# Kernel optimization log

Measured on AMD Instinct MI355X. Metric: run time of the kernel, lower is better.

Reference implementation:

```python
import jax, jax.numpy as jnp
import numpy as np

SIGMA = 1.0
DELTA = 1.0
TOPK = 10
TOPK_HALF = int(np.around(TOPK / 2))  # 5
EPS = 1e-12


def _cdist(a, b):
    # Euclidean distance matrix, grad-safe sqrt at zero (matches torch.cdist values).
    d2 = (jnp.sum(a * a, axis=1)[:, None]
          + jnp.sum(b * b, axis=1)[None, :]
          - 2.0 * (a @ b.T))
    d2 = jnp.maximum(d2, 0.0)
    pos = d2 > 0.0
    return jnp.where(pos, jnp.sqrt(jnp.where(pos, d2, 1.0)), 0.0)


def _consistency_weights(t_emb):
    # Everything here is under torch.no_grad() in the original.
    N = t_emb.shape[0]
    T_dist = _cdist(t_emb, t_emb)
    W_P = jnp.exp(-(T_dist ** 2) / SIGMA)
    _, idx = jax.lax.top_k(W_P, TOPK)                      # [N, TOPK]
    rows = jnp.arange(N)[:, None]
    W_NN = jnp.zeros_like(W_P).at[rows, idx].set(1.0)      # scatter_ ones
    V = (((W_NN + W_NN.T) / 2) == 1.0).astype(W_P.dtype)   # mutual kNN (symmetric)
    # Vectorized form of the per-row python loop:
    #   W_C_tilda[i, j] = V[i, j] * (sum_k V[i, k] * V[j, k]) / sum_k V[i, k]
    deg = jnp.sum(V, axis=1)                               # >= 1 (self is always a NN)
    overlap = V @ V.T                                      # [N, N] neighbor overlap
    W_C_tilda = V * overlap / deg[:, None]
    topk_half_index = idx[:, :TOPK_HALF]                   # [N, TOPK_HALF]
    W_C_hat = jnp.mean(W_C_tilda[topk_half_index], axis=1) # gather rows, mean -> [N, N]
    W_C = (W_C_hat + W_C_hat.T) / 2
    return (W_P + W_C) / 2


def reference(s_emb, t_emb):
    # disable_mu = 0 -> s_emb NOT normalized; t_emb always normalized.
    t_norm = t_emb / jnp.maximum(
        jnp.linalg.norm(t_emb, axis=1, keepdims=True), EPS)
    N = s_emb.shape[0]
    S_dist = _cdist(s_emb, s_emb)
    S_dist = S_dist / jnp.mean(S_dist, axis=1, keepdims=True)
    W = jax.lax.stop_gradient(_consistency_weights(t_norm))
    off_diag = 1.0 - jnp.eye(N, dtype=W.dtype)
    pos_weight = W * off_diag
    neg_weight = (1.0 - W) * off_diag
    pull = jnp.maximum(S_dist, 0.0) ** 2 * pos_weight
    push = jnp.maximum(DELTA - S_dist, 0.0) ** 2 * neg_weight
    return (jnp.sum(pull) + jnp.sum(push)) / (N * (N - 1))


def setup_inputs() -> dict:
    key = jax.random.key(0)
    k1, k2 = jax.random.split(key)
    N, D = 2048, 1024
    return {
        "s_emb": jax.random.normal(k1, (N, D), dtype=jnp.float32),
        "t_emb": jax.random.normal(k2, (N, D), dtype=jnp.float32),
    }
```

## Files before the change

### kernel.cpp

```cpp
#include <hip/hip_runtime.h>
#include <math.h>

#define N_ 2048
#define D_ 1024
#define TOPK 10
#define TOPK_HALF 5
#define INV_NORM (1.0f / ((float)N_ * (float)(N_ - 1)))

typedef __attribute__((ext_vector_type(8))) short short8;
typedef __attribute__((ext_vector_type(4))) float floatx4;

__device__ __forceinline__ short f2bf(float f) {
  unsigned u = __float_as_uint(f);
  unsigned r = (u + 0x7fffu + ((u >> 16) & 1u)) >> 16;
  return (short)r;
}
__device__ __forceinline__ float bf2f(short b) {
  return __uint_as_float(((unsigned)(unsigned short)b) << 16);
}

__device__ __forceinline__ void gld_lds16(const short* g, short* l) {
  __builtin_amdgcn_global_load_lds(
      (const __attribute__((address_space(1))) unsigned int*)(g),
      (__attribute__((address_space(3))) unsigned int*)(l), 16, 0, 0);
}

#define BAR() asm volatile("s_barrier" ::: "memory")
#define WAIT4_BAR() asm volatile("s_waitcnt vmcnt(4)\ns_barrier" ::: "memory")
#define WAIT0_BAR() asm volatile("s_waitcnt vmcnt(0)\ns_barrier" ::: "memory")

__global__ __launch_bounds__(256) void prep_kernel(const float* __restrict__ t,
                                                   const float* __restrict__ s,
                                                   short* __restrict__ tb,
                                                   short* __restrict__ sb,
                                                   float* __restrict__ tt,
                                                   float* __restrict__ ss,
                                                   float* __restrict__ rowsum,
                                                   float* __restrict__ out) {
  int b = blockIdx.x, tid = threadIdx.x;
  __shared__ float red[256];
  if (b == 0) {
    for (int j = tid; j < N_; j += 256) rowsum[j] = 0.f;
    if (tid == 0) out[0] = 0.f;
  }
  if (b < N_) {
    const float4* rp = (const float4*)(t + (size_t)b * D_);
    float4 v = rp[tid];
    red[tid] = v.x * v.x + v.y * v.y + v.z * v.z + v.w * v.w;
    __syncthreads();
    for (int st = 128; st > 0; st >>= 1) { if (tid < st) red[tid] += red[tid + st]; __syncthreads(); }
    float inv = 1.f / fmaxf(sqrtf(red[0]), 1e-12f);
    __syncthreads();
    float a = v.x * inv, bb = v.y * inv, c = v.z * inv, d = v.w * inv;
    uint2 pk;
    pk.x = (unsigned)(unsigned short)f2bf(a) | ((unsigned)(unsigned short)f2bf(bb) << 16);
    pk.y = (unsigned)(unsigned short)f2bf(c) | ((unsigned)(unsigned short)f2bf(d) << 16);
    ((uint2*)(tb + (size_t)b * D_))[tid] = pk;
    red[tid] = a * a + bb * bb + c * c + d * d;
    __syncthreads();
    for (int st = 128; st > 0; st >>= 1) { if (tid < st) red[tid] += red[tid + st]; __syncthreads(); }
    if (tid == 0) tt[b] = red[0];
  } else {
    int row = b - N_;
    const float4* rp = (const float4*)(s + (size_t)row * D_);
    float4 v = rp[tid];
    uint2 pk;
    pk.x = (unsigned)(unsigned short)f2bf(v.x) | ((unsigned)(unsigned short)f2bf(v.y) << 16);
    pk.y = (unsigned)(unsigned short)f2bf(v.z) | ((unsigned)(unsigned short)f2bf(v.w) << 16);
    ((uint2*)(sb + (size_t)row * D_))[tid] = pk;
    red[tid] = v.x * v.x + v.y * v.y + v.z * v.z + v.w * v.w;
    __syncthreads();
    for (int st = 128; st > 0; st >>= 1) { if (tid < st) red[tid] += red[tid + st]; __syncthreads(); }
    if (tid == 0) ss[row] = red[0];
  }
}

#define NTRI 528
__global__ __launch_bounds__(256) void gram_sym_kernel(
    const short* __restrict__ Tb, const short* __restrict__ Sb,
    const float* __restrict__ tt, const float* __restrict__ ss,
    short* __restrict__ WPb, short* __restrict__ Sob,
    float* __restrict__ rowsum) {
  int p = blockIdx.x;
  const int mode = (p >= NTRI);
  int q = p - mode * NTRI;
  int bi = (int)((sqrtf(8.f * (float)q + 1.f) - 1.f) * 0.5f);
  if (bi > 31) bi = 31;
  while ((bi + 1) * (bi + 2) / 2 <= q) bi++;
  while (bi * (bi + 1) / 2 > q) bi--;
  int bj = q - bi * (bi + 1) / 2;

  const short* A = mode ? Sb : Tb;
  const float* rn = mode ? ss : tt;
  short* outb = mode ? Sob : WPb;

  __shared__ __align__(16) short smem[4 * 4096];

  int tid = threadIdx.x;
  int w = tid >> 6, lane = tid & 63;
  int i0 = bi * 64, j0 = bj * 64;
  int wr = w >> 1, wc = w & 1;
  int quad = lane >> 4, l16 = lane & 15;

  floatx4 acc[2][2] = {};

  int sr8 = lane >> 3;
  int gch = ((lane & 7) ^ sr8) * 8;
  const short* Ag = A + (size_t)(i0 + w * 16 + sr8) * D_ + gch;
  const short* Bg = A + (size_t)(j0 + w * 16 + sr8) * D_ + gch;
  int lloc = (w * 16 + sr8) * 64 + (lane & 7) * 8;

#define STAGE(buf, k0)                                                   \
  do {                                                                   \
    short* Al = smem + (buf)*8192 + lloc;                                \
    short* Bl = smem + (buf)*8192 + 4096 + lloc;                         \
    gld_lds16(Ag + (k0), Al);                                            \
    gld_lds16(Ag + (k0) + (size_t)8 * D_, Al + 512);                     \
    gld_lds16(Bg + (k0), Bl);                                            \
    gld_lds16(Bg + (k0) + (size_t)8 * D_, Bl + 512);                     \
  } while (0)

  STAGE(0, 0);
#pragma unroll 2
  for (int it = 0; it < 16; it++) {
    int cur = it & 1;
    if (it) BAR();
    if (it < 15) {
      STAGE(!cur, (it + 1) * 64);
      WAIT4_BAR();
    } else {
      WAIT0_BAR();
    }
    const short* Ab = smem + cur * 8192;
    const short* Bb = smem + cur * 8192 + 4096;
#pragma unroll
    for (int ks = 0; ks < 64; ks += 32) {
      int cb = ks >> 3;
      short8 af[2], bfr[2];
#pragma unroll
      for (int mt = 0; mt < 2; mt++) {
        int rr = wr * 32 + mt * 16 + l16;
        af[mt] = *(const short8*)&Ab[rr * 64 + (((cb + quad) ^ (l16 & 7)) << 3)];
      }
#pragma unroll
      for (int nt = 0; nt < 2; nt++) {
        int rr = wc * 32 + nt * 16 + l16;
        bfr[nt] = *(const short8*)&Bb[rr * 64 + (((cb + quad) ^ (l16 & 7)) << 3)];
      }
#pragma unroll
      for (int mt = 0; mt < 2; mt++)
#pragma unroll
        for (int nt = 0; nt < 2; nt++)
          acc[mt][nt] = __builtin_amdgcn_mfma_f32_16x16x32_bf16(af[mt], bfr[nt], acc[mt][nt], 0, 0, 0);
    }
  }

  float ov[2][2][4];
#pragma unroll
  for (int mt = 0; mt < 2; mt++) {
#pragma unroll
    for (int r = 0; r < 4; r++) {
      int i = i0 + wr * 32 + mt * 16 + quad * 4 + r;
      float ri = rn[i];
      float rs = 0.f;
#pragma unroll
      for (int nt = 0; nt < 2; nt++) {
        int j = j0 + wc * 32 + nt * 16 + l16;
        float d2 = fmaxf(ri + rn[j] - 2.f * acc[mt][nt][r], 0.f);
        float o = mode ? sqrtf(d2) : expf(-d2);
        if (i == j) o = mode ? 0.f : 1.f;
        ov[mt][nt][r] = o;
        outb[(size_t)i * N_ + j] = f2bf(o);
        rs += o;
      }
      if (mode) {
        rs += __shfl_xor(rs, 1); rs += __shfl_xor(rs, 2);
        rs += __shfl_xor(rs, 4); rs += __shfl_xor(rs, 8);
        if (l16 == 0) atomicAdd(&rowsum[i], rs);
      }
    }
  }

  if (bi != bj) {
    if (mode) {
#pragma unroll
      for (int nt = 0; nt < 2; nt++) {
        float cs = 0.f;
#pragma unroll
        for (int mt = 0; mt < 2; mt++)
#pragma unroll
          for (int r = 0; r < 4; r++) cs += ov[mt][nt][r];
        cs += __shfl_xor(cs, 16);
        cs += __shfl_xor(cs, 32);
        if (quad == 0) atomicAdd(&rowsum[j0 + wc * 32 + nt * 16 + l16], cs);
      }
    }
    BAR();
    float* fs = (float*)smem + w * 1088;
#pragma unroll
    for (int mt = 0; mt < 2; mt++)
#pragma unroll
      for (int nt = 0; nt < 2; nt++)
#pragma unroll
        for (int r = 0; r < 4; r++) {
          int lr = mt * 16 + quad * 4 + r;
          int lc = nt * 16 + l16;
          fs[lc * 34 + lr] = ov[mt][nt][r];
        }
#pragma unroll
    for (int itx = 0; itx < 8; itx++) {
      int sidx = itx * 64 + lane;
      int lc = sidx >> 4;
      int k2 = (sidx & 15) * 2;
      float lo = fs[lc * 34 + k2];
      float hi = fs[lc * 34 + k2 + 1];
      unsigned pk = (unsigned)(unsigned short)f2bf(lo) |
                    ((unsigned)(unsigned short)f2bf(hi) << 16);
      size_t jg = (size_t)(j0 + wc * 32 + lc);
      *(unsigned*)(outb + jg * N_ + i0 + wr * 32 + k2) = pk;
    }
  }
}

__global__ __launch_bounds__(64) void topk_loss_kernel(const short* __restrict__ WPb,
                                                       const short* __restrict__ Sb,
                                                       const float* __restrict__ rowsum,
                                                       int* __restrict__ idx,
                                                       unsigned* __restrict__ mask,
                                                       float* __restrict__ out) {
  int row = blockIdx.x, lane = threadIdx.x;
  const short8* wpr = (const short8*)(WPb + (size_t)row * N_);
  const short8* sr = (const short8*)(Sb + (size_t)row * N_);
  float rminv = (float)N_ / rowsum[row];
  float w[32];
  float local = 0.f;
#pragma unroll
  for (int c4 = 0; c4 < 4; c4++) {
    short8 wp8 = wpr[lane * 4 + c4];
    short8 s8 = sr[lane * 4 + c4];
#pragma unroll
    for (int e = 0; e < 8; e++) {
      float wv = bf2f(wp8[e]);
      w[c4 * 8 + e] = wv;
      float sv = bf2f(s8[e]) * rminv;
      float d = fmaxf(1.f - sv, 0.f);
      local += d * d + 0.5f * wv * (sv * sv - d * d);
    }
  }
#pragma unroll
  for (int off = 32; off > 0; off >>= 1) local += __shfl_down(local, off);
  if (lane == 0) {
    atomicAdd(out, (local - 0.5f) * INV_NORM);
    mask[row] = 0u;
  }
  int base = lane * 32;
  int sel[TOPK];
  for (int t = 0; t < TOPK; t++) {
    float bv = -2.f; int bi = 0;
#pragma unroll
    for (int c = 0; c < 32; c++)
      if (w[c] > bv) { bv = w[c]; bi = base + c; }
#pragma unroll
    for (int off = 32; off > 0; off >>= 1) {
      float ovv = __shfl_down(bv, off);
      int oi = __shfl_down(bi, off);
      if (ovv > bv || (ovv == bv && oi < bi)) { bv = ovv; bi = oi; }
    }
    bi = __shfl(bi, 0);
    sel[t] = bi;
    bool mine = (bi >> 5) == lane;
    int cc = bi & 31;
#pragma unroll
    for (int c = 0; c < 32; c++)
      if (mine && cc == c) w[c] = -1.f;
  }
  if (lane == 0) {
#pragma unroll
    for (int t = 0; t < TOPK; t++) idx[row * TOPK + t] = sel[t];
  }
}

__global__ __launch_bounds__(256) void mutual_kernel(const int* __restrict__ idx,
                                                     unsigned* __restrict__ mask) {
  int t = blockIdx.x * 256 + threadIdx.x;
  int i = t >> 4, k = t & 15;
  if (i >= N_ || k >= TOPK) return;
  int j = idx[i * TOPK + k];
  bool mut = false;
#pragma unroll
  for (int l = 0; l < TOPK; l++) mut |= (idx[j * TOPK + l] == i);
  if (mut) atomicOr(&mask[i], 1u << k);
}

__global__ __launch_bounds__(256) void sparse_wc_kernel(
    const int* __restrict__ idx, const unsigned* __restrict__ mask,
    const short* __restrict__ Sb, const float* __restrict__ rowsum,
    float* __restrict__ out) {
  int t = blockIdx.x * 256 + threadIdx.x;
  int i = t >> 6, r = t & 63;
  float contrib = 0.f;
  if (i < N_ && r < TOPK_HALF * TOPK) {
    int mi = r / TOPK, k = r - mi * TOPK;
    int m = idx[i * TOPK + mi];
    unsigned mm = mask[m];
    if ((mm >> k) & 1u) {
      int col = idx[m * TOPK + k];
      if (col != i) {
        int dm = __popc(mm);
        unsigned mc = mask[col];
        int jm[TOPK], jc[TOPK];
#pragma unroll
        for (int l = 0; l < TOPK; l++) jm[l] = idx[m * TOPK + l];
#pragma unroll
        for (int l = 0; l < TOPK; l++) jc[l] = idx[col * TOPK + l];
        int c = 0;
#pragma unroll
        for (int a = 0; a < TOPK; a++) {
          if ((mm >> a) & 1u) {
            int na = jm[a];
#pragma unroll
            for (int b = 0; b < TOPK; b++) c += (((mc >> b) & 1u) && (jc[b] == na));
          }
        }
        float v = (float)c / (float)dm * 0.1f;
        float s1 = bf2f(Sb[(size_t)i * N_ + col]) * ((float)N_ / rowsum[i]);
        float d1 = fmaxf(1.f - s1, 0.f);
        float s2 = bf2f(Sb[(size_t)col * N_ + i]) * ((float)N_ / rowsum[col]);
        float d2 = fmaxf(1.f - s2, 0.f);
        contrib = 0.5f * v * ((s1 * s1 - d1 * d1) + (s2 * s2 - d2 * d2));
      }
    }
  }
  __shared__ float red[256];
  red[threadIdx.x] = contrib; __syncthreads();
  for (int st = 128; st > 0; st >>= 1) {
    if (threadIdx.x < st) red[threadIdx.x] += red[threadIdx.x + st];
    __syncthreads();
  }
  if (threadIdx.x == 0) atomicAdd(out, red[0] * INV_NORM);
}

extern "C" void kernel_launch(void* const* d_in, const int* in_sizes, int n_in,
                              void* d_out, int out_size, void* d_ws, size_t ws_size,
                              hipStream_t stream) {
  const float* s_emb = (const float*)d_in[0];
  const float* t_emb = (const float*)d_in[1];
  float* out = (float*)d_out;

  const size_t NN = (size_t)N_ * N_;
  const size_t ND = (size_t)N_ * D_;
  short* t_bf = (short*)d_ws;
  short* s_bf = t_bf + ND;
  short* WPb = s_bf + ND;
  short* Sb = WPb + NN;
  float* tt = (float*)(Sb + NN);
  float* ss = tt + N_;
  float* rowsum = ss + N_;
  int* idx = (int*)(rowsum + N_);
  unsigned* mask = (unsigned*)(idx + (size_t)N_ * TOPK);

  prep_kernel<<<2 * N_, 256, 0, stream>>>(t_emb, s_emb, t_bf, s_bf, tt, ss, rowsum, out);

  gram_sym_kernel<<<2 * NTRI, 256, 0, stream>>>(t_bf, s_bf, tt, ss, WPb, Sb, rowsum);

  topk_loss_kernel<<<N_, 64, 0, stream>>>(WPb, Sb, rowsum, idx, mask, out);
  mutual_kernel<<<N_ * 16 / 256, 256, 0, stream>>>(idx, mask);
  sparse_wc_kernel<<<N_ * 64 / 256, 256, 0, stream>>>(idx, mask, Sb, rowsum, out);
}
```

Baseline: 141.3 us.

## Fuse all stages into one cooperative persistent kernel with grid syncs

Replaces the five separate launches (prep, symmetric gram, topk/loss, mutual, sparse WC) with a single cooperative kernel that loops over the work of each phase and separates phases with grid.sync. The prep phase now uses one wave per row with shuffle reductions instead of shared-memory tree reductions. The aim is to remove per-launch overhead and the tail gaps between kernels. In exchange it caps the grid at up to 1024 blocks, adds the cost of the grid barriers, and leaves the topk phase using only 2 of 4 waves per block.

```diff
diff --git a/kernel.cpp b/kernel.cpp
--- a/kernel.cpp
+++ b/kernel.cpp
@@ -1,10 +1,14 @@
 #include <hip/hip_runtime.h>
+#include <hip/hip_cooperative_groups.h>
 #include <math.h>
+
+namespace cg = cooperative_groups;
 
 #define N_ 2048
 #define D_ 1024
 #define TOPK 10
 #define TOPK_HALF 5
+#define NTRI 528
 #define INV_NORM (1.0f / ((float)N_ * (float)(N_ - 1)))
 
 typedef __attribute__((ext_vector_type(8))) short short8;
@@ -29,315 +33,315 @@
 #define WAIT4_BAR() asm volatile("s_waitcnt vmcnt(4)\ns_barrier" ::: "memory")
 #define WAIT0_BAR() asm volatile("s_waitcnt vmcnt(0)\ns_barrier" ::: "memory")
 
-__global__ __launch_bounds__(256) void prep_kernel(const float* __restrict__ t,
-                                                   const float* __restrict__ s,
-                                                   short* __restrict__ tb,
-                                                   short* __restrict__ sb,
-                                                   float* __restrict__ tt,
-                                                   float* __restrict__ ss,
-                                                   float* __restrict__ rowsum,
-                                                   float* __restrict__ out) {
-  int b = blockIdx.x, tid = threadIdx.x;
-  __shared__ float red[256];
-  if (b == 0) {
+__global__ __launch_bounds__(256, 4) void mega_kernel(
+    const float* __restrict__ t, const float* __restrict__ s,
+    short* __restrict__ tb, short* __restrict__ sb,
+    float* __restrict__ tt, float* __restrict__ ss,
+    float* __restrict__ rowsum, int* __restrict__ idx,
+    unsigned* __restrict__ mask,
+    short* __restrict__ WPb, short* __restrict__ Sob,
+    float* __restrict__ out) {
+  cg::grid_group grid = cg::this_grid();
+  __shared__ __align__(16) short smem[4 * 4096];
+  int tid = threadIdx.x, w = tid >> 6, lane = tid & 63;
+
+  if (blockIdx.x == 0) {
     for (int j = tid; j < N_; j += 256) rowsum[j] = 0.f;
     if (tid == 0) out[0] = 0.f;
   }
-  if (b < N_) {
-    const float4* rp = (const float4*)(t + (size_t)b * D_);
-    float4 v = rp[tid];
-    red[tid] = v.x * v.x + v.y * v.y + v.z * v.z + v.w * v.w;
+  if (blockIdx.x == 1 % gridDim.x) {
+    for (int j = tid; j < N_; j += 256) mask[j] = 0u;
+  }
+  for (int row = blockIdx.x * 4 + w; row < 2 * N_; row += gridDim.x * 4) {
+    if (row < N_) {
+      const float4* rp = (const float4*)(t + (size_t)row * D_);
+      float4 v[4];
+      float acc = 0.f;
+#pragma unroll
+      for (int c4 = 0; c4 < 4; c4++) {
+        v[c4] = rp[lane + 64 * c4];
+        acc += v[c4].x * v[c4].x + v[c4].y * v[c4].y + v[c4].z * v[c4].z + v[c4].w * v[c4].w;
+      }
+#pragma unroll
+      for (int off = 1; off < 64; off <<= 1) acc += __shfl_xor(acc, off);
+      float inv = 1.f / fmaxf(sqrtf(acc), 1e-12f);
+      float s2 = 0.f;
+#pragma unroll
+      for (int c4 = 0; c4 < 4; c4++) {
+        float a = v[c4].x * inv, b = v[c4].y * inv, c = v[c4].z * inv, d = v[c4].w * inv;
+        uint2 pk;
+        pk.x = (unsigned)(unsigned short)f2bf(a) | ((unsigned)(unsigned short)f2bf(b) << 16);
+        pk.y = (unsigned)(unsigned short)f2bf(c) | ((unsigned)(unsigned short)f2bf(d) << 16);
+        ((uint2*)(tb + (size_t)row * D_))[lane + 64 * c4] = pk;
+        s2 += a * a + b * b + c * c + d * d;
+      }
+#pragma unroll
+      for (int off = 1; off < 64; off <<= 1) s2 += __shfl_xor(s2, off);
+      if (lane == 0) tt[row] = s2;
+    } else {
+      int r2 = row - N_;
+      const float4* rp = (const float4*)(s + (size_t)r2 * D_);
+      float acc = 0.f;
+#pragma unroll
+      for (int c4 = 0; c4 < 4; c4++) {
+        float4 v = rp[lane + 64 * c4];
+        uint2 pk;
+        pk.x = (unsigned)(unsigned short)f2bf(v.x) | ((unsigned)(unsigned short)f2bf(v.y) << 16);
+        pk.y = (unsigned)(unsigned short)f2bf(v.z) | ((unsigned)(unsigned short)f2bf(v.w) << 16);
+        ((uint2*)(sb + (size_t)r2 * D_))[lane + 64 * c4] = pk;
+        acc += v.x * v.x + v.y * v.y + v.z * v.z + v.w * v.w;
+      }
+#pragma unroll
+      for (int off = 1; off < 64; off <<= 1) acc += __shfl_xor(acc, off);
+      if (lane == 0) ss[r2] = acc;
+    }
+  }
+  grid.sync();
+
+  for (int p = blockIdx.x; p < 2 * NTRI; p += gridDim.x) {
     __syncthreads();
-    for (int st = 128; st > 0; st >>= 1) { if (tid < st) red[tid] += red[tid + st]; __syncthreads(); }
-    float inv = 1.f / fmaxf(sqrtf(red[0]), 1e-12f);
+    const int mode = (p >= NTRI);
+    int q = p - mode * NTRI;
+    int bi = (int)((sqrtf(8.f * (float)q + 1.f) - 1.f) * 0.5f);
+    if (bi > 31) bi = 31;
+    while ((bi + 1) * (bi + 2) / 2 <= q) bi++;
+    while (bi * (bi + 1) / 2 > q) bi--;
+    int bj = q - bi * (bi + 1) / 2;
+
+    const short* A = mode ? sb : tb;
+    const float* rn = mode ? ss : tt;
+    short* outb = mode ? Sob : WPb;
+
+    int i0 = bi * 64, j0 = bj * 64;
+    int wr = w >> 1, wc = w & 1;
+    int quad = lane >> 4, l16 = lane & 15;
+    floatx4 acc[2][2] = {};
+
+    int sr8 = lane >> 3;
+    int gch = ((lane & 7) ^ sr8) * 8;
+    const short* Ag = A + (size_t)(i0 + w * 16 + sr8) * D_ + gch;
+    const short* Bg = A + (size_t)(j0 + w * 16 + sr8) * D_ + gch;
+    int lloc = (w * 16 + sr8) * 64 + (lane & 7) * 8;
+
+#define STAGE(buf, k0)                                       \
+  do {                                                       \
+    short* Al = smem + (buf)*8192 + lloc;                    \
+    short* Bl = smem + (buf)*8192 + 4096 + lloc;             \
+    gld_lds16(Ag + (k0), Al);                                \
+    gld_lds16(Ag + (k0) + (size_t)8 * D_, Al + 512);         \
+    gld_lds16(Bg + (k0), Bl);                                \
+    gld_lds16(Bg + (k0) + (size_t)8 * D_, Bl + 512);         \
+  } while (0)
+
+    STAGE(0, 0);
+#pragma unroll 2
+    for (int it = 0; it < 16; it++) {
+      int cur = it & 1;
+      if (it) BAR();
+      if (it < 15) {
+        STAGE(!cur, (it + 1) * 64);
+        WAIT4_BAR();
+      } else {
+        WAIT0_BAR();
+      }
+      const short* Ab = smem + cur * 8192;
+      const short* Bb = smem + cur * 8192 + 4096;
+#pragma unroll
+      for (int ks = 0; ks < 64; ks += 32) {
+        int cb = ks >> 3;
+        short8 af[2], bfr[2];
+#pragma unroll
+        for (int mt = 0; mt < 2; mt++) {
+          int rr = wr * 32 + mt * 16 + l16;
+          af[mt] = *(const short8*)&Ab[rr * 64 + (((cb + quad) ^ (l16 & 7)) << 3)];
+        }
+#pragma unroll
+        for (int nt = 0; nt < 2; nt++) {
+          int rr = wc * 32 + nt * 16 + l16;
+          bfr[nt] = *(const short8*)&Bb[rr * 64 + (((cb + quad) ^ (l16 & 7)) << 3)];
+        }
+#pragma unroll
+        for (int mt = 0; mt < 2; mt++)
+#pragma unroll
+          for (int nt = 0; nt < 2; nt++)
+            acc[mt][nt] = __builtin_amdgcn_mfma_f32_16x16x32_bf16(af[mt], bfr[nt], acc[mt][nt], 0, 0, 0);
+      }
+    }
+
+    float ov[2][2][4];
+#pragma unroll
+    for (int mt = 0; mt < 2; mt++) {
+#pragma unroll
+      for (int r = 0; r < 4; r++) {
+        int i = i0 + wr * 32 + mt * 16 + quad * 4 + r;
+        float ri = rn[i];
+        float rs = 0.f;
+#pragma unroll
+        for (int nt = 0; nt < 2; nt++) {
+          int j = j0 + wc * 32 + nt * 16 + l16;
+          float d2 = fmaxf(ri + rn[j] - 2.f * acc[mt][nt][r], 0.f);
+          float o = mode ? sqrtf(d2) : expf(-d2);
+          if (i == j) o = mode ? 0.f : 1.f;
+          ov[mt][nt][r] = o;
+          outb[(size_t)i * N_ + j] = f2bf(o);
+          rs += o;
+        }
+        if (mode) {
+          rs += __shfl_xor(rs, 1); rs += __shfl_xor(rs, 2);
+          rs += __shfl_xor(rs, 4); rs += __shfl_xor(rs, 8);
+          if (l16 == 0) atomicAdd(&rowsum[i], rs);
+        }
+      }
+    }
+
+    if (bi != bj) {
+      if (mode) {
+#pragma unroll
+        for (int nt = 0; nt < 2; nt++) {
+          float cs = 0.f;
+#pragma unroll
+          for (int mt = 0; mt < 2; mt++)
+#pragma unroll
+            for (int r = 0; r < 4; r++) cs += ov[mt][nt][r];
+          cs += __shfl_xor(cs, 16);
+          cs += __shfl_xor(cs, 32);
+          if (quad == 0) atomicAdd(&rowsum[j0 + wc * 32 + nt * 16 + l16], cs);
+        }
+      }
+      BAR();
+      float* fs = (float*)smem + w * 1088;
+#pragma unroll
+      for (int mt = 0; mt < 2; mt++)
+#pragma unroll
+        for (int nt = 0; nt < 2; nt++)
+#pragma unroll
+          for (int r = 0; r < 4; r++)
+            fs[(nt * 16 + l16) * 34 + mt * 16 + quad * 4 + r] = ov[mt][nt][r];
+#pragma unroll
+      for (int itx = 0; itx < 8; itx++) {
+        int sidx = itx * 64 + lane;
+        int lc = sidx >> 4;
+        int k2 = (sidx & 15) * 2;
+        float lo = fs[lc * 34 + k2];
+        float hi = fs[lc * 34 + k2 + 1];
+        unsigned pk = (unsigned)(unsigned short)f2bf(lo) |
+                      ((unsigned)(unsigned short)f2bf(hi) << 16);
+        size_t jg = (size_t)(j0 + wc * 32 + lc);
+        *(unsigned*)(outb + jg * N_ + i0 + wr * 32 + k2) = pk;
+      }
+    }
+  }
+  grid.sync();
+
+  if (w < 2) {
+    for (int row = blockIdx.x * 2 + w; row < N_; row += gridDim.x * 2) {
+      const short8* wpr = (const short8*)(WPb + (size_t)row * N_);
+      const short8* sr = (const short8*)(Sob + (size_t)row * N_);
+      float rminv = (float)N_ / rowsum[row];
+      float wreg[32];
+      float local = 0.f;
+#pragma unroll
+      for (int c4 = 0; c4 < 4; c4++) {
+        short8 wp8 = wpr[lane * 4 + c4];
+        short8 s8 = sr[lane * 4 + c4];
+#pragma unroll
+        for (int e = 0; e < 8; e++) {
+          float wv = bf2f(wp8[e]);
+          wreg[c4 * 8 + e] = wv;
+          float sv = bf2f(s8[e]) * rminv;
+          float d = fmaxf(1.f - sv, 0.f);
+          local += d * d + 0.5f * wv * (sv * sv - d * d);
+        }
+      }
+#pragma unroll
+      for (int off = 32; off > 0; off >>= 1) local += __shfl_down(local, off);
+      if (lane == 0) atomicAdd(out, (local - 0.5f) * INV_NORM);
+      int base = lane * 32;
+      int sel[TOPK];
+      for (int tq = 0; tq < TOPK; tq++) {
+        float bv = -2.f; int bi = 0;
+#pragma unroll
+        for (int c = 0; c < 32; c++)
+          if (wreg[c] > bv) { bv = wreg[c]; bi = base + c; }
+#pragma unroll
+        for (int off = 32; off > 0; off >>= 1) {
+          float ovv = __shfl_down(bv, off);
+          int oi = __shfl_down(bi, off);
+          if (ovv > bv || (ovv == bv && oi < bi)) { bv = ovv; bi = oi; }
+        }
+        bi = __shfl(bi, 0);
+        sel[tq] = bi;
+        bool mine = (bi >> 5) == lane;
+        int cc = bi & 31;
+#pragma unroll
+        for (int c = 0; c < 32; c++)
+          if (mine && cc == c) wreg[c] = -1.f;
+      }
+      if (lane == 0) {
+#pragma unroll
+        for (int tq = 0; tq < TOPK; tq++) idx[row * TOPK + tq] = sel[tq];
+      }
+    }
+  }
+  grid.sync();
+
+  for (int tk = blockIdx.x * 256 + tid; tk < N_ * 16; tk += gridDim.x * 256) {
+    int i = tk >> 4, k = tk & 15;
+    if (k < TOPK) {
+      int j = idx[i * TOPK + k];
+      bool mut = false;
+#pragma unroll
+      for (int l = 0; l < TOPK; l++) mut |= (idx[j * TOPK + l] == i);
+      if (mut) atomicOr(&mask[i], 1u << k);
+    }
+  }
+  grid.sync();
+
+  float contrib = 0.f;
+  for (int tk = blockIdx.x * 256 + tid; tk < N_ * 64; tk += gridDim.x * 256) {
+    int i = tk >> 6, r = tk & 63;
+    if (r < TOPK_HALF * TOPK) {
+      int mi = r / TOPK, k = r - mi * TOPK;
+      int m = idx[i * TOPK + mi];
+      unsigned mm = mask[m];
+      if ((mm >> k) & 1u) {
+        int col = idx[m * TOPK + k];
+        if (col != i) {
+          int dm = __popc(mm);
+          unsigned mc = mask[col];
+          int jm[TOPK], jc[TOPK];
+#pragma unroll
+          for (int l = 0; l < TOPK; l++) jm[l] = idx[m * TOPK + l];
+#pragma unroll
+          for (int l = 0; l < TOPK; l++) jc[l] = idx[col * TOPK + l];
+          int c = 0;
+#pragma unroll
+          for (int a = 0; a < TOPK; a++) {
+            if ((mm >> a) & 1u) {
+              int na = jm[a];
+#pragma unroll
+              for (int b = 0; b < TOPK; b++) c += (((mc >> b) & 1u) && (jc[b] == na));
+            }
+          }
+          float v = (float)c / (float)dm * 0.1f;
+          float s1 = bf2f(Sob[(size_t)i * N_ + col]) * ((float)N_ / rowsum[i]);
+          float d1 = fmaxf(1.f - s1, 0.f);
+          float s2 = bf2f(Sob[(size_t)col * N_ + i]) * ((float)N_ / rowsum[col]);
+          float d2 = fmaxf(1.f - s2, 0.f);
+          contrib += 0.5f * v * ((s1 * s1 - d1 * d1) + (s2 * s2 - d2 * d2));
+        }
+      }
+    }
+  }
+  __syncthreads();
+  float* red = (float*)smem;
+  red[tid] = contrib;
+  __syncthreads();
+  for (int st = 128; st > 0; st >>= 1) {
+    if (tid < st) red[tid] += red[tid + st];
     __syncthreads();
-    float a = v.x * inv, bb = v.y * inv, c = v.z * inv, d = v.w * inv;
-    uint2 pk;
-    pk.x = (unsigned)(unsigned short)f2bf(a) | ((unsigned)(unsigned short)f2bf(bb) << 16);
-    pk.y = (unsigned)(unsigned short)f2bf(c) | ((unsigned)(unsigned short)f2bf(d) << 16);
-    ((uint2*)(tb + (size_t)b * D_))[tid] = pk;
-    red[tid] = a * a + bb * bb + c * c + d * d;
-    __syncthreads();
-    for (int st = 128; st > 0; st >>= 1) { if (tid < st) red[tid] += red[tid + st]; __syncthreads(); }
-    if (tid == 0) tt[b] = red[0];
-  } else {
-    int row = b - N_;
-    const float4* rp = (const float4*)(s + (size_t)row * D_);
-    float4 v = rp[tid];
-    uint2 pk;
-    pk.x = (unsigned)(unsigned short)f2bf(v.x) | ((unsigned)(unsigned short)f2bf(v.y) << 16);
-    pk.y = (unsigned)(unsigned short)f2bf(v.z) | ((unsigned)(unsigned short)f2bf(v.w) << 16);
-    ((uint2*)(sb + (size_t)row * D_))[tid] = pk;
-    red[tid] = v.x * v.x + v.y * v.y + v.z * v.z + v.w * v.w;
-    __syncthreads();
-    for (int st = 128; st > 0; st >>= 1) { if (tid < st) red[tid] += red[tid + st]; __syncthreads(); }
-    if (tid == 0) ss[row] = red[0];
-  }
-}
-
-#define NTRI 528
-__global__ __launch_bounds__(256) void gram_sym_kernel(
-    const short* __restrict__ Tb, const short* __restrict__ Sb,
-    const float* __restrict__ tt, const float* __restrict__ ss,
-    short* __restrict__ WPb, short* __restrict__ Sob,
-    float* __restrict__ rowsum) {
-  int p = blockIdx.x;
-  const int mode = (p >= NTRI);
-  int q = p - mode * NTRI;
-  int bi = (int)((sqrtf(8.f * (float)q + 1.f) - 1.f) * 0.5f);
-  if (bi > 31) bi = 31;
-  while ((bi + 1) * (bi + 2) / 2 <= q) bi++;
-  while (bi * (bi + 1) / 2 > q) bi--;
-  int bj = q - bi * (bi + 1) / 2;
-
-  const short* A = mode ? Sb : Tb;
-  const float* rn = mode ? ss : tt;
-  short* outb = mode ? Sob : WPb;
-
-  __shared__ __align__(16) short smem[4 * 4096];
-
-  int tid = threadIdx.x;
-  int w = tid >> 6, lane = tid & 63;
-  int i0 = bi * 64, j0 = bj * 64;
-  int wr = w >> 1, wc = w & 1;
-  int quad = lane >> 4, l16 = lane & 15;
-
-  floatx4 acc[2][2] = {};
-
-  int sr8 = lane >> 3;
-  int gch = ((lane & 7) ^ sr8) * 8;
-  const short* Ag = A + (size_t)(i0 + w * 16 + sr8) * D_ + gch;
-  const short* Bg = A + (size_t)(j0 + w * 16 + sr8) * D_ + gch;
-  int lloc = (w * 16 + sr8) * 64 + (lane & 7) * 8;
-
-#define STAGE(buf, k0)                                                   \
-  do {                                                                   \
-    short* Al = smem + (buf)*8192 + lloc;                                \
-    short* Bl = smem + (buf)*8192 + 4096 + lloc;                         \
-    gld_lds16(Ag + (k0), Al);                                            \
-    gld_lds16(Ag + (k0) + (size_t)8 * D_, Al + 512);                     \
-    gld_lds16(Bg + (k0), Bl);                                            \
-    gld_lds16(Bg + (k0) + (size_t)8 * D_, Bl + 512);                     \
-  } while (0)
-
-  STAGE(0, 0);
-#pragma unroll 2
-  for (int it = 0; it < 16; it++) {
-    int cur = it & 1;
-    if (it) BAR();
-    if (it < 15) {
-      STAGE(!cur, (it + 1) * 64);
-      WAIT4_BAR();
-    } else {
-      WAIT0_BAR();
-    }
-    const short* Ab = smem + cur * 8192;
-    const short* Bb = smem + cur * 8192 + 4096;
-#pragma unroll
-    for (int ks = 0; ks < 64; ks += 32) {
-      int cb = ks >> 3;
-      short8 af[2], bfr[2];
-#pragma unroll
-      for (int mt = 0; mt < 2; mt++) {
-        int rr = wr * 32 + mt * 16 + l16;
-        af[mt] = *(const short8*)&Ab[rr * 64 + (((cb + quad) ^ (l16 & 7)) << 3)];
-      }
-#pragma unroll
-      for (int nt = 0; nt < 2; nt++) {
-        int rr = wc * 32 + nt * 16 + l16;
-        bfr[nt] = *(const short8*)&Bb[rr * 64 + (((cb + quad) ^ (l16 & 7)) << 3)];
-      }
-#pragma unroll
-      for (int mt = 0; mt < 2; mt++)
-#pragma unroll
-        for (int nt = 0; nt < 2; nt++)
-          acc[mt][nt] = __builtin_amdgcn_mfma_f32_16x16x32_bf16(af[mt], bfr[nt], acc[mt][nt], 0, 0, 0);
-    }
-  }
-
-  float ov[2][2][4];
-#pragma unroll
-  for (int mt = 0; mt < 2; mt++) {
-#pragma unroll
-    for (int r = 0; r < 4; r++) {
-      int i = i0 + wr * 32 + mt * 16 + quad * 4 + r;
-      float ri = rn[i];
-      float rs = 0.f;
-#pragma unroll
-      for (int nt = 0; nt < 2; nt++) {
-        int j = j0 + wc * 32 + nt * 16 + l16;
-        float d2 = fmaxf(ri + rn[j] - 2.f * acc[mt][nt][r], 0.f);
-        float o = mode ? sqrtf(d2) : expf(-d2);
-        if (i == j) o = mode ? 0.f : 1.f;
-        ov[mt][nt][r] = o;
-        outb[(size_t)i * N_ + j] = f2bf(o);
-        rs += o;
-      }
-      if (mode) {
-        rs += __shfl_xor(rs, 1); rs += __shfl_xor(rs, 2);
-        rs += __shfl_xor(rs, 4); rs += __shfl_xor(rs, 8);
-        if (l16 == 0) atomicAdd(&rowsum[i], rs);
-      }
-    }
-  }
-
-  if (bi != bj) {
-    if (mode) {
-#pragma unroll
-      for (int nt = 0; nt < 2; nt++) {
-        float cs = 0.f;
-#pragma unroll
-        for (int mt = 0; mt < 2; mt++)
-#pragma unroll
-          for (int r = 0; r < 4; r++) cs += ov[mt][nt][r];
-        cs += __shfl_xor(cs, 16);
-        cs += __shfl_xor(cs, 32);
-        if (quad == 0) atomicAdd(&rowsum[j0 + wc * 32 + nt * 16 + l16], cs);
-      }
-    }
-    BAR();
-    float* fs = (float*)smem + w * 1088;
-#pragma unroll
-    for (int mt = 0; mt < 2; mt++)
-#pragma unroll
-      for (int nt = 0; nt < 2; nt++)
-#pragma unroll
-        for (int r = 0; r < 4; r++) {
-          int lr = mt * 16 + quad * 4 + r;
-          int lc = nt * 16 + l16;
-          fs[lc * 34 + lr] = ov[mt][nt][r];
-        }
-#pragma unroll
-    for (int itx = 0; itx < 8; itx++) {
-      int sidx = itx * 64 + lane;
-      int lc = sidx >> 4;
-      int k2 = (sidx & 15) * 2;
-      float lo = fs[lc * 34 + k2];
-      float hi = fs[lc * 34 + k2 + 1];
-      unsigned pk = (unsigned)(unsigned short)f2bf(lo) |
-                    ((unsigned)(unsigned short)f2bf(hi) << 16);
-      size_t jg = (size_t)(j0 + wc * 32 + lc);
-      *(unsigned*)(outb + jg * N_ + i0 + wr * 32 + k2) = pk;
-    }
-  }
-}
-
-__global__ __launch_bounds__(64) void topk_loss_kernel(const short* __restrict__ WPb,
-                                                       const short* __restrict__ Sb,
-                                                       const float* __restrict__ rowsum,
-                                                       int* __restrict__ idx,
-                                                       unsigned* __restrict__ mask,
-                                                       float* __restrict__ out) {
-  int row = blockIdx.x, lane = threadIdx.x;
-  const short8* wpr = (const short8*)(WPb + (size_t)row * N_);
-  const short8* sr = (const short8*)(Sb + (size_t)row * N_);
-  float rminv = (float)N_ / rowsum[row];
-  float w[32];
-  float local = 0.f;
-#pragma unroll
-  for (int c4 = 0; c4 < 4; c4++) {
-    short8 wp8 = wpr[lane * 4 + c4];
-    short8 s8 = sr[lane * 4 + c4];
-#pragma unroll
-    for (int e = 0; e < 8; e++) {
-      float wv = bf2f(wp8[e]);
-      w[c4 * 8 + e] = wv;
-      float sv = bf2f(s8[e]) * rminv;
-      float d = fmaxf(1.f - sv, 0.f);
-      local += d * d + 0.5f * wv * (sv * sv - d * d);
-    }
-  }
-#pragma unroll
-  for (int off = 32; off > 0; off >>= 1) local += __shfl_down(local, off);
-  if (lane == 0) {
-    atomicAdd(out, (local - 0.5f) * INV_NORM);
-    mask[row] = 0u;
-  }
-  int base = lane * 32;
-  int sel[TOPK];
-  for (int t = 0; t < TOPK; t++) {
-    float bv = -2.f; int bi = 0;
-#pragma unroll
-    for (int c = 0; c < 32; c++)
-      if (w[c] > bv) { bv = w[c]; bi = base + c; }
-#pragma unroll
-    for (int off = 32; off > 0; off >>= 1) {
-      float ovv = __shfl_down(bv, off);
-      int oi = __shfl_down(bi, off);
-      if (ovv > bv || (ovv == bv && oi < bi)) { bv = ovv; bi = oi; }
-    }
-    bi = __shfl(bi, 0);
-    sel[t] = bi;
-    bool mine = (bi >> 5) == lane;
-    int cc = bi & 31;
-#pragma unroll
-    for (int c = 0; c < 32; c++)
-      if (mine && cc == c) w[c] = -1.f;
-  }
-  if (lane == 0) {
-#pragma unroll
-    for (int t = 0; t < TOPK; t++) idx[row * TOPK + t] = sel[t];
-  }
-}
-
-__global__ __launch_bounds__(256) void mutual_kernel(const int* __restrict__ idx,
-                                                     unsigned* __restrict__ mask) {
-  int t = blockIdx.x * 256 + threadIdx.x;
-  int i = t >> 4, k = t & 15;
-  if (i >= N_ || k >= TOPK) return;
-  int j = idx[i * TOPK + k];
-  bool mut = false;
-#pragma unroll
-  for (int l = 0; l < TOPK; l++) mut |= (idx[j * TOPK + l] == i);
-  if (mut) atomicOr(&mask[i], 1u << k);
-}
-
-__global__ __launch_bounds__(256) void sparse_wc_kernel(
-    const int* __restrict__ idx, const unsigned* __restrict__ mask,
-    const short* __restrict__ Sb, const float* __restrict__ rowsum,
-    float* __restrict__ out) {
-  int t = blockIdx.x * 256 + threadIdx.x;
-  int i = t >> 6, r = t & 63;
-  float contrib = 0.f;
-  if (i < N_ && r < TOPK_HALF * TOPK) {
-    int mi = r / TOPK, k = r - mi * TOPK;
-    int m = idx[i * TOPK + mi];
-    unsigned mm = mask[m];
-    if ((mm >> k) & 1u) {
-      int col = idx[m * TOPK + k];
-      if (col != i) {
-        int dm = __popc(mm);
-        unsigned mc = mask[col];
-        int jm[TOPK], jc[TOPK];
-#pragma unroll
-        for (int l = 0; l < TOPK; l++) jm[l] = idx[m * TOPK + l];
-#pragma unroll
-        for (int l = 0; l < TOPK; l++) jc[l] = idx[col * TOPK + l];
-        int c = 0;
-#pragma unroll
-        for (int a = 0; a < TOPK; a++) {
-          if ((mm >> a) & 1u) {
-            int na = jm[a];
-#pragma unroll
-            for (int b = 0; b < TOPK; b++) c += (((mc >> b) & 1u) && (jc[b] == na));
-          }
-        }
-        float v = (float)c / (float)dm * 0.1f;
-        float s1 = bf2f(Sb[(size_t)i * N_ + col]) * ((float)N_ / rowsum[i]);
-        float d1 = fmaxf(1.f - s1, 0.f);
-        float s2 = bf2f(Sb[(size_t)col * N_ + i]) * ((float)N_ / rowsum[col]);
-        float d2 = fmaxf(1.f - s2, 0.f);
-        contrib = 0.5f * v * ((s1 * s1 - d1 * d1) + (s2 * s2 - d2 * d2));
-      }
-    }
-  }
-  __shared__ float red[256];
-  red[threadIdx.x] = contrib; __syncthreads();
-  for (int st = 128; st > 0; st >>= 1) {
-    if (threadIdx.x < st) red[threadIdx.x] += red[threadIdx.x + st];
-    __syncthreads();
-  }
-  if (threadIdx.x == 0) atomicAdd(out, red[0] * INV_NORM);
+  }
+  if (tid == 0) atomicAdd(out, red[0] * INV_NORM);
 }
 
 extern "C" void kernel_launch(void* const* d_in, const int* in_sizes, int n_in,
@@ -359,11 +363,14 @@
   int* idx = (int*)(rowsum + N_);
   unsigned* mask = (unsigned*)(idx + (size_t)N_ * TOPK);
 
-  prep_kernel<<<2 * N_, 256, 0, stream>>>(t_emb, s_emb, t_bf, s_bf, tt, ss, rowsum, out);
-
-  gram_sym_kernel<<<2 * NTRI, 256, 0, stream>>>(t_bf, s_bf, tt, ss, WPb, Sb, rowsum);
-
-  topk_loss_kernel<<<N_, 64, 0, stream>>>(WPb, Sb, rowsum, idx, mask, out);
-  mutual_kernel<<<N_ * 16 / 256, 256, 0, stream>>>(idx, mask);
-  sparse_wc_kernel<<<N_ * 64 / 256, 256, 0, stream>>>(idx, mask, Sb, rowsum, out);
-}
+  int nb = 4;
+  hipOccupancyMaxActiveBlocksPerMultiprocessor(&nb, mega_kernel, 256, 0);
+  int grid = nb * 256;
+  if (grid > 1024) grid = 1024;
+  if (grid < 256) grid = 256;
+
+  void* args[] = {(void*)&t_emb, (void*)&s_emb, (void*)&t_bf, (void*)&s_bf,
+                  (void*)&tt,    (void*)&ss,    (void*)&rowsum, (void*)&idx,
+                  (void*)&mask,  (void*)&WPb,   (void*)&Sb,     (void*)&out};
+  hipLaunchCooperativeKernel((void*)mega_kernel, dim3(grid), dim3(256), args, 0, stream);
+}
```

New measurement: 348.2 us. +146.4%, slower.

## Use 32x32x16 MFMA in gram kernel and fuse mutual-mask into sparse kernel

Applied to the files above, without the earlier changes.

The gram kernel's inner product switches from four 16x16x32 bf16 MFMAs per wave to a single 32x32x16 MFMA accumulator, which halves the LDS fragment loads and reshapes the epilogue, the row/column sum reductions and the transpose store around the new register layout. Separately, the mutual-kNN kernel launch is removed. Each sparse_wc thread now recomputes the mutual masks for m and col directly from idx. This saves a launch and a global mask array in exchange for redundant index reads and compares, and the row-sum reduction now needs more shuffles per register.

```diff
diff --git a/kernel.cpp b/kernel.cpp
--- a/kernel.cpp
+++ b/kernel.cpp
@@ -5,10 +5,11 @@
 #define D_ 1024
 #define TOPK 10
 #define TOPK_HALF 5
+#define NTRI 528
 #define INV_NORM (1.0f / ((float)N_ * (float)(N_ - 1)))
 
 typedef __attribute__((ext_vector_type(8))) short short8;
-typedef __attribute__((ext_vector_type(4))) float floatx4;
+typedef __attribute__((ext_vector_type(16))) float floatx16;
 
 __device__ __forceinline__ short f2bf(float f) {
   unsigned u = __float_as_uint(f);
@@ -75,7 +76,6 @@
   }
 }
 
-#define NTRI 528
 __global__ __launch_bounds__(256) void gram_sym_kernel(
     const short* __restrict__ Tb, const short* __restrict__ Sb,
     const float* __restrict__ tt, const float* __restrict__ ss,
@@ -100,9 +100,9 @@
   int w = tid >> 6, lane = tid & 63;
   int i0 = bi * 64, j0 = bj * 64;
   int wr = w >> 1, wc = w & 1;
-  int quad = lane >> 4, l16 = lane & 15;
-
-  floatx4 acc[2][2] = {};
+  int l32 = lane & 31, half = lane >> 5;
+
+  floatx16 acc = {};
 
   int sr8 = lane >> 3;
   int gch = ((lane & 7) ^ sr8) * 8;
@@ -110,14 +110,14 @@
   const short* Bg = A + (size_t)(j0 + w * 16 + sr8) * D_ + gch;
   int lloc = (w * 16 + sr8) * 64 + (lane & 7) * 8;
 
-#define STAGE(buf, k0)                                                   \
-  do {                                                                   \
-    short* Al = smem + (buf)*8192 + lloc;                                \
-    short* Bl = smem + (buf)*8192 + 4096 + lloc;                         \
-    gld_lds16(Ag + (k0), Al);                                            \
-    gld_lds16(Ag + (k0) + (size_t)8 * D_, Al + 512);                     \
-    gld_lds16(Bg + (k0), Bl);                                            \
-    gld_lds16(Bg + (k0) + (size_t)8 * D_, Bl + 512);                     \
+#define STAGE(buf, k0)                                       \
+  do {                                                       \
+    short* Al = smem + (buf)*8192 + lloc;                    \
+    short* Bl = smem + (buf)*8192 + 4096 + lloc;             \
+    gld_lds16(Ag + (k0), Al);                                \
+    gld_lds16(Ag + (k0) + (size_t)8 * D_, Al + 512);         \
+    gld_lds16(Bg + (k0), Bl);                                \
+    gld_lds16(Bg + (k0) + (size_t)8 * D_, Bl + 512);         \
   } while (0)
 
   STAGE(0, 0);
@@ -134,79 +134,56 @@
     const short* Ab = smem + cur * 8192;
     const short* Bb = smem + cur * 8192 + 4096;
 #pragma unroll
-    for (int ks = 0; ks < 64; ks += 32) {
-      int cb = ks >> 3;
-      short8 af[2], bfr[2];
-#pragma unroll
-      for (int mt = 0; mt < 2; mt++) {
-        int rr = wr * 32 + mt * 16 + l16;
-        af[mt] = *(const short8*)&Ab[rr * 64 + (((cb + quad) ^ (l16 & 7)) << 3)];
-      }
-#pragma unroll
-      for (int nt = 0; nt < 2; nt++) {
-        int rr = wc * 32 + nt * 16 + l16;
-        bfr[nt] = *(const short8*)&Bb[rr * 64 + (((cb + quad) ^ (l16 & 7)) << 3)];
-      }
-#pragma unroll
-      for (int mt = 0; mt < 2; mt++)
-#pragma unroll
-        for (int nt = 0; nt < 2; nt++)
-          acc[mt][nt] = __builtin_amdgcn_mfma_f32_16x16x32_bf16(af[mt], bfr[nt], acc[mt][nt], 0, 0, 0);
-    }
-  }
-
-  float ov[2][2][4];
-#pragma unroll
-  for (int mt = 0; mt < 2; mt++) {
-#pragma unroll
-    for (int r = 0; r < 4; r++) {
-      int i = i0 + wr * 32 + mt * 16 + quad * 4 + r;
-      float ri = rn[i];
-      float rs = 0.f;
-#pragma unroll
-      for (int nt = 0; nt < 2; nt++) {
-        int j = j0 + wc * 32 + nt * 16 + l16;
-        float d2 = fmaxf(ri + rn[j] - 2.f * acc[mt][nt][r], 0.f);
-        float o = mode ? sqrtf(d2) : expf(-d2);
-        if (i == j) o = mode ? 0.f : 1.f;
-        ov[mt][nt][r] = o;
-        outb[(size_t)i * N_ + j] = f2bf(o);
-        rs += o;
-      }
-      if (mode) {
-        rs += __shfl_xor(rs, 1); rs += __shfl_xor(rs, 2);
-        rs += __shfl_xor(rs, 4); rs += __shfl_xor(rs, 8);
-        if (l16 == 0) atomicAdd(&rowsum[i], rs);
+    for (int kstep = 0; kstep < 4; kstep++) {
+      int cA = (((2 * kstep + half) ^ (l32 & 7)) << 3);
+      short8 af = *(const short8*)&Ab[(wr * 32 + l32) * 64 + cA];
+      short8 bfr = *(const short8*)&Bb[(wc * 32 + l32) * 64 + cA];
+      acc = __builtin_amdgcn_mfma_f32_32x32x16_bf16(af, bfr, acc, 0, 0, 0);
+    }
+  }
+
+  float ov[16];
+  int jcol = j0 + wc * 32 + l32;
+  float rj = rn[jcol];
+#pragma unroll
+  for (int reg = 0; reg < 16; reg++) {
+    int rl = (reg & 3) + 8 * (reg >> 2) + 4 * half;
+    int i = i0 + wr * 32 + rl;
+    float d2 = fmaxf(rn[i] + rj - 2.f * acc[reg], 0.f);
+    float o = mode ? sqrtf(d2) : expf(-d2);
+    if (i == jcol) o = mode ? 0.f : 1.f;
+    ov[reg] = o;
+    outb[(size_t)i * N_ + jcol] = f2bf(o);
+  }
+  if (mode) {
+#pragma unroll
+    for (int reg = 0; reg < 16; reg++) {
+      float rs = ov[reg];
+      rs += __shfl_xor(rs, 1); rs += __shfl_xor(rs, 2);
+      rs += __shfl_xor(rs, 4); rs += __shfl_xor(rs, 8);
+      rs += __shfl_xor(rs, 16);
+      if (l32 == 0) {
+        int rl = (reg & 3) + 8 * (reg >> 2) + 4 * half;
+        atomicAdd(&rowsum[i0 + wr * 32 + rl], rs);
       }
     }
   }
 
   if (bi != bj) {
     if (mode) {
-#pragma unroll
-      for (int nt = 0; nt < 2; nt++) {
-        float cs = 0.f;
-#pragma unroll
-        for (int mt = 0; mt < 2; mt++)
-#pragma unroll
-          for (int r = 0; r < 4; r++) cs += ov[mt][nt][r];
-        cs += __shfl_xor(cs, 16);
-        cs += __shfl_xor(cs, 32);
-        if (quad == 0) atomicAdd(&rowsum[j0 + wc * 32 + nt * 16 + l16], cs);
-      }
+      float cs = 0.f;
+#pragma unroll
+      for (int reg = 0; reg < 16; reg++) cs += ov[reg];
+      cs += __shfl_xor(cs, 32);
+      if (half == 0) atomicAdd(&rowsum[jcol], cs);
     }
     BAR();
     float* fs = (float*)smem + w * 1088;
 #pragma unroll
-    for (int mt = 0; mt < 2; mt++)
-#pragma unroll
-      for (int nt = 0; nt < 2; nt++)
-#pragma unroll
-        for (int r = 0; r < 4; r++) {
-          int lr = mt * 16 + quad * 4 + r;
-          int lc = nt * 16 + l16;
-          fs[lc * 34 + lr] = ov[mt][nt][r];
-        }
+    for (int reg = 0; reg < 16; reg++) {
+      int rl = (reg & 3) + 8 * (reg >> 2) + 4 * half;
+      fs[l32 * 34 + rl] = ov[reg];
+    }
 #pragma unroll
     for (int itx = 0; itx < 8; itx++) {
       int sidx = itx * 64 + lane;
@@ -226,7 +203,6 @@
                                                        const short* __restrict__ Sb,
                                                        const float* __restrict__ rowsum,
                                                        int* __restrict__ idx,
-                                                       unsigned* __restrict__ mask,
                                                        float* __restrict__ out) {
   int row = blockIdx.x, lane = threadIdx.x;
   const short8* wpr = (const short8*)(WPb + (size_t)row * N_);
@@ -249,10 +225,7 @@
   }
 #pragma unroll
   for (int off = 32; off > 0; off >>= 1) local += __shfl_down(local, off);
-  if (lane == 0) {
-    atomicAdd(out, (local - 0.5f) * INV_NORM);
-    mask[row] = 0u;
-  }
+  if (lane == 0) atomicAdd(out, (local - 0.5f) * INV_NORM);
   int base = lane * 32;
   int sel[TOPK];
   for (int t = 0; t < TOPK; t++) {
@@ -280,34 +253,37 @@
   }
 }
 
-__global__ __launch_bounds__(256) void mutual_kernel(const int* __restrict__ idx,
-                                                     unsigned* __restrict__ mask) {
-  int t = blockIdx.x * 256 + threadIdx.x;
-  int i = t >> 4, k = t & 15;
-  if (i >= N_ || k >= TOPK) return;
-  int j = idx[i * TOPK + k];
-  bool mut = false;
-#pragma unroll
-  for (int l = 0; l < TOPK; l++) mut |= (idx[j * TOPK + l] == i);
-  if (mut) atomicOr(&mask[i], 1u << k);
+__device__ __forceinline__ unsigned mutual_mask(const int* __restrict__ idx, int x) {
+  unsigned m = 0;
+  int nb[TOPK];
+#pragma unroll
+  for (int k = 0; k < TOPK; k++) nb[k] = idx[x * TOPK + k];
+#pragma unroll
+  for (int k = 0; k < TOPK; k++) {
+    int j = nb[k];
+    bool mut = false;
+#pragma unroll
+    for (int l = 0; l < TOPK; l++) mut |= (idx[j * TOPK + l] == x);
+    if (mut) m |= 1u << k;
+  }
+  return m;
 }
 
 __global__ __launch_bounds__(256) void sparse_wc_kernel(
-    const int* __restrict__ idx, const unsigned* __restrict__ mask,
-    const short* __restrict__ Sb, const float* __restrict__ rowsum,
-    float* __restrict__ out) {
+    const int* __restrict__ idx, const short* __restrict__ Sb,
+    const float* __restrict__ rowsum, float* __restrict__ out) {
   int t = blockIdx.x * 256 + threadIdx.x;
   int i = t >> 6, r = t & 63;
   float contrib = 0.f;
   if (i < N_ && r < TOPK_HALF * TOPK) {
     int mi = r / TOPK, k = r - mi * TOPK;
     int m = idx[i * TOPK + mi];
-    unsigned mm = mask[m];
+    unsigned mm = mutual_mask(idx, m);
     if ((mm >> k) & 1u) {
       int col = idx[m * TOPK + k];
       if (col != i) {
         int dm = __popc(mm);
-        unsigned mc = mask[col];
+        unsigned mc = mutual_mask(idx, col);
         int jm[TOPK], jc[TOPK];
 #pragma unroll
         for (int l = 0; l < TOPK; l++) jm[l] = idx[m * TOPK + l];
@@ -357,13 +333,11 @@
   float* ss = tt + N_;
   float* rowsum = ss + N_;
   int* idx = (int*)(rowsum + N_);
-  unsigned* mask = (unsigned*)(idx + (size_t)N_ * TOPK);
 
   prep_kernel<<<2 * N_, 256, 0, stream>>>(t_emb, s_emb, t_bf, s_bf, tt, ss, rowsum, out);
 
   gram_sym_kernel<<<2 * NTRI, 256, 0, stream>>>(t_bf, s_bf, tt, ss, WPb, Sb, rowsum);
 
-  topk_loss_kernel<<<N_, 64, 0, stream>>>(WPb, Sb, rowsum, idx, mask, out);
-  mutual_kernel<<<N_ * 16 / 256, 256, 0, stream>>>(idx, mask);
-  sparse_wc_kernel<<<N_ * 64 / 256, 256, 0, stream>>>(idx, mask, Sb, rowsum, out);
-}
+  topk_loss_kernel<<<N_, 64, 0, stream>>>(WPb, Sb, rowsum, idx, out);
+  sparse_wc_kernel<<<N_ * 64 / 256, 256, 0, stream>>>(idx, Sb, rowsum, out);
+}
```

Measured after the change: 151.2 us. 6.9% more time.
